# Performance work log

Hardware: AMD Instinct MI355X
Metric: run time of the kernel (lower is better)

## Reference

```python
import jax, jax.numpy as jnp
import numpy as np

EMBED_DIM = 2048
NUM_HEADS = 32
NUM_KV_HEADS = 8
HEAD_DIM = EMBED_DIM // NUM_HEADS  # 64
KV_DIM = HEAD_DIM * NUM_KV_HEADS   # 512
Q_PER_KV = NUM_HEADS // NUM_KV_HEADS  # 4


def setup_inputs() -> dict:
    key = jax.random.key(0)
    ks = jax.random.split(key, 9)
    s = 1.0 / np.sqrt(EMBED_DIM)
    x = jax.random.normal(ks[0], (2, 2048, EMBED_DIM), dtype=jnp.float32)
    Wq = jax.random.uniform(ks[1], (EMBED_DIM, EMBED_DIM), jnp.float32, -s, s)
    bq = jax.random.uniform(ks[2], (EMBED_DIM,), jnp.float32, -s, s)
    Wk = jax.random.uniform(ks[3], (KV_DIM, EMBED_DIM), jnp.float32, -s, s)
    bk = jax.random.uniform(ks[4], (KV_DIM,), jnp.float32, -s, s)
    Wv = jax.random.uniform(ks[5], (KV_DIM, EMBED_DIM), jnp.float32, -s, s)
    bv = jax.random.uniform(ks[6], (KV_DIM,), jnp.float32, -s, s)
    Wo = jax.random.uniform(ks[7], (EMBED_DIM, EMBED_DIM), jnp.float32, -s, s)
    bo = jax.random.uniform(ks[8], (EMBED_DIM,), jnp.float32, -s, s)
    return {"x": x, "Wq": Wq, "bq": bq, "Wk": Wk, "bk": bk,
            "Wv": Wv, "bv": bv, "Wo": Wo, "bo": bo}


def reference(x, Wq, bq, Wk, bk, Wv, bv, Wo, bo):
    B, S, E = x.shape
    # projections (torch Linear: x @ W.T + b)
    q = x @ Wq.T + bq                       # [B,S,E]
    k = x @ Wk.T + bk                       # [B,S,KV_DIM]
    v = x @ Wv.T + bv
    # [B, num_kv, q_per_kv, S, D] and [B, num_kv, S, D] -- GQA grouping
    # avoids repeat_interleave duplication while computing identical math
    q = q.reshape(B, S, NUM_KV_HEADS, Q_PER_KV, HEAD_DIM).transpose(0, 2, 3, 1, 4)
    k = k.reshape(B, S, NUM_KV_HEADS, HEAD_DIM).transpose(0, 2, 1, 3)
    v = v.reshape(B, S, NUM_KV_HEADS, HEAD_DIM).transpose(0, 2, 1, 3)
    scale = 1.0 / np.sqrt(HEAD_DIM).astype(np.float32)
    scores = jnp.einsum('bgqsd,bgtd->bgqst', q, k) * scale  # [B,G,Qpk,S,S]
    causal = jnp.triu(jnp.ones((S, S), dtype=bool), k=1)
    scores = jnp.where(causal, jnp.float32(-jnp.inf), scores)
    attn = jax.nn.softmax(scores, axis=-1)
    out = jnp.einsum('bgqst,bgtd->bgqsd', attn, v)          # [B,G,Qpk,S,D]
    # back to [B,S,E]: head order matches repeat_interleave (kv-major)
    out = out.transpose(0, 3, 1, 2, 4).reshape(B, S, E)
    return out @ Wo.T + bo
```

## Files before the change

kernel.cpp:

```cpp
#include <hip/hip_runtime.h>
#include <stdint.h>

#define EMBED  2048
#define SEQ    2048
#define BATCH  2
#define NHEADS 32
#define NKV    8
#define HDIM   64
#define KVD    512
#define MTOT   (BATCH*SEQ)
#define QKVN   (EMBED + 2*KVD)

typedef __bf16 bf16x8 __attribute__((ext_vector_type(8)));
typedef float  f32x4  __attribute__((ext_vector_type(4)));
typedef float  f32x8v __attribute__((ext_vector_type(8)));
typedef float  f32x2v __attribute__((ext_vector_type(2)));
typedef float  f32x16 __attribute__((ext_vector_type(16)));

#define QSCALE 0.18033688f
#define M2     11.541560f

static __device__ __forceinline__ unsigned short f2bf(float f) {
    union { float f; unsigned int u; } v; v.f = f;
    return (unsigned short)((v.u + 0x7fffu + ((v.u >> 16) & 1u)) >> 16);
}

static __device__ __forceinline__ void gload_lds16(const void* g, void* l) {
    __builtin_amdgcn_global_load_lds(
        (const __attribute__((address_space(1))) void*)g,
        (__attribute__((address_space(3))) void*)l, 16, 0, 0);
}

template<int N> static __device__ __forceinline__ void waitvm() {
    if constexpr (N == 2) asm volatile("s_waitcnt vmcnt(2)" ::: "memory");
    else if constexpr (N == 3) asm volatile("s_waitcnt vmcnt(3)" ::: "memory");
    else asm volatile("s_waitcnt vmcnt(4)" ::: "memory");
}

static __device__ __forceinline__ void cast4(const float* __restrict__ in,
                                             unsigned short* __restrict__ out, int i) {
    float4 f = reinterpret_cast<const float4*>(in)[i];
    ushort4 o;
    o.x = f2bf(f.x); o.y = f2bf(f.y); o.z = f2bf(f.z); o.w = f2bf(f.w);
    reinterpret_cast<ushort4*>(out)[i] = o;
}

__global__ __launch_bounds__(256)
void prep(const float* __restrict__ x,  const float* __restrict__ Wq,
          const float* __restrict__ Wk, const float* __restrict__ Wv,
          const float* __restrict__ Wo, const float* __restrict__ bq,
          const float* __restrict__ bk, const float* __restrict__ bv,
          unsigned short* __restrict__ xb, unsigned short* __restrict__ Wqkvb,
          unsigned short* __restrict__ Wob, float* __restrict__ bqkv)
{
    const int t0 = blockIdx.x * blockDim.x + threadIdx.x;
    const int st = gridDim.x * blockDim.x;
    for (int i = t0; i < (MTOT * EMBED) / 4;  i += st) cast4(x,  xb, i);
    for (int i = t0; i < (EMBED * EMBED) / 4; i += st) cast4(Wq, Wqkvb, i);
    for (int i = t0; i < (KVD * EMBED) / 4;   i += st) cast4(Wk, Wqkvb + EMBED * EMBED, i);
    for (int i = t0; i < (KVD * EMBED) / 4;   i += st) cast4(Wv, Wqkvb + (EMBED + KVD) * EMBED, i);
    for (int i = t0; i < (EMBED * EMBED) / 4; i += st) cast4(Wo, Wob, i);
    if (t0 < QKVN / 4) {
        float4 v = (t0 < EMBED / 4) ? reinterpret_cast<const float4*>(bq)[t0]
                 : (t0 < (EMBED + KVD) / 4) ? reinterpret_cast<const float4*>(bk)[t0 - EMBED / 4]
                 : reinterpret_cast<const float4*>(bv)[t0 - (EMBED + KVD) / 4];
        reinterpret_cast<float4*>(bqkv)[t0] = v;
    }
}

template<int WM, bool OUT_BF16>
__global__ __launch_bounds__(512, 1)
void gemm8p(const unsigned short* __restrict__ A,
            const unsigned short* __restrict__ B,
            const float* __restrict__ bias,
            void* __restrict__ C, int M, int N, int K)
{
    constexpr int BM    = WM * 32;
    constexpr int ASZ   = BM * 128;
    constexpr int BSZ   = 256 * 128;
    constexpr int AHALF = ASZ / 2;
    constexpr int AL    = AHALF / 8192;
    constexpr int BUFSZ = ASZ + BSZ;

    __shared__ __align__(16) char lds[2 * BUFSZ];

    const int tid = threadIdx.x;
    const int l   = tid & 63;
    const int w   = tid >> 6;
    const int wr  = w >> 2, wc = w & 3;
    const int lr15 = l & 15;
    const int lkb  = (l >> 4) * 16;

    const int nwg = gridDim.x;
    const int cpx = nwg >> 3;
    const int bid = blockIdx.x;
    const int swz = (bid & 7) * cpx + (bid >> 3);
    const int NMB = M / BM;
    const int m0  = (swz % NMB) * BM;
    const int n0  = (swz / NMB) * 256;

    unsigned offA[2][AL], dA[2][AL];
#pragma unroll
    for (int q = 0; q < 2; ++q)
#pragma unroll
        for (int j = 0; j < AL; ++j) {
            int L  = q * AHALF + (tid + j * 512) * 16;
            int R  = L >> 7;
            int cb = (L & 127) ^ ((R & 7) << 4);
            int lrow;
            if constexpr (WM == 8) lrow = ((R >> 6) & 1) * 128 + (R >> 7) * 64 + (R & 63);
            else                   lrow = ((R >> 5) & 1) * 64  + (R >> 6) * 32 + (R & 31);
            offA[q][j] = (unsigned)((m0 + lrow) * K * 2 + cb);
            dA[q][j]   = (unsigned)L;
        }
    unsigned offB[2][2], dB[2][2];
#pragma unroll
    for (int q = 0; q < 2; ++q)
#pragma unroll
        for (int j = 0; j < 2; ++j) {
            int L  = q * 16384 + (tid + j * 512) * 16;
            int R  = L >> 7;
            int cb = (L & 127) ^ ((R & 7) << 4);
            int lrow = ((R >> 5) & 3) * 64 + (R >> 7) * 32 + (R & 31);
            offB[q][j] = (unsigned)((n0 + lrow) * K * 2 + cb);
            dB[q][j]   = (unsigned)(ASZ + L);
        }

#define STAGE_A(q, bw, ku) { _Pragma("unroll") \
    for (int j_ = 0; j_ < AL; ++j_) \
        gload_lds16((const char*)A + offA[q][j_] + (unsigned)(ku) * 128u, (bw) + dA[q][j_]); }
#define STAGE_B(q, bw, ku) { _Pragma("unroll") \
    for (int j_ = 0; j_ < 2; ++j_) \
        gload_lds16((const char*)B + offB[q][j_] + (unsigned)(ku) * 128u, (bw) + dB[q][j_]); }

    auto rdA = [&](const char* br, int mi, int kk) -> bf16x8 {
        int row;
        if constexpr (WM == 8) row = (mi >> 2) * 128 + wr * 64 + (mi & 3) * 16 + lr15;
        else                   row = (mi >> 1) * 64  + wr * 32 + (mi & 1) * 16 + lr15;
        int byte = (row * 128 + kk * 64 + lkb) ^ ((row & 7) << 4);
        return *reinterpret_cast<const bf16x8*>(br + byte);
    };
    auto rdB = [&](const char* br, int ni, int kk) -> bf16x8 {
        int row  = (ni >> 1) * 128 + wc * 32 + (ni & 1) * 16 + lr15;
        int byte = (row * 128 + kk * 64 + lkb) ^ ((row & 7) << 4);
        return *reinterpret_cast<const bf16x8*>(br + ASZ + byte);
    };

    f32x4 acc[WM][4] = {};
    bf16x8 afr[WM / 2][2], bf0[2][2], bf1[2][2];

    STAGE_A(0, lds, 0); STAGE_B(0, lds, 0); STAGE_B(1, lds, 0); STAGE_A(1, lds, 0);
    waitvm<2 + AL>();
    __builtin_amdgcn_s_barrier();

    const int NKT = K >> 6;
    for (int u = 0; u < NKT; ++u) {
        char* br = lds + (u & 1) * BUFSZ;
        char* bw = lds + ((u & 1) ^ 1) * BUFSZ;
        const bool pf = (u + 1 < NKT);
        const int  ku = u + 1;

        if (pf) STAGE_A(0, bw, ku);
#pragma unroll
        for (int mi = 0; mi < WM / 2; ++mi)
#pragma unroll
            for (int kk = 0; kk < 2; ++kk) afr[mi][kk] = rdA(br, mi, kk);
#pragma unroll
        for (int ni = 0; ni < 2; ++ni)
#pragma unroll
            for (int kk = 0; kk < 2; ++kk) bf0[ni][kk] = rdB(br, ni, kk);
        __builtin_amdgcn_s_barrier();
        __builtin_amdgcn_s_setprio(1);
#pragma unroll
        for (int mi = 0; mi < WM / 2; ++mi)
#pragma unroll
            for (int ni = 0; ni < 2; ++ni)
#pragma unroll
                for (int kk = 0; kk < 2; ++kk)
                    acc[mi][ni] = __builtin_amdgcn_mfma_f32_16x16x32_bf16(afr[mi][kk], bf0[ni][kk], acc[mi][ni], 0, 0, 0);
        __builtin_amdgcn_s_setprio(0);
        waitvm<2 * AL>();
        __builtin_amdgcn_s_barrier();

        if (pf) STAGE_B(0, bw, ku);
#pragma unroll
        for (int ni = 0; ni < 2; ++ni)
#pragma unroll
            for (int kk = 0; kk < 2; ++kk) bf1[ni][kk] = rdB(br, 2 + ni, kk);
        __builtin_amdgcn_s_barrier();
        __builtin_amdgcn_s_setprio(1);
#pragma unroll
        for (int mi = 0; mi < WM / 2; ++mi)
#pragma unroll
            for (int ni = 0; ni < 2; ++ni)
#pragma unroll
                for (int kk = 0; kk < 2; ++kk)
                    acc[mi][2 + ni] = __builtin_amdgcn_mfma_f32_16x16x32_bf16(afr[mi][kk], bf1[ni][kk], acc[mi][2 + ni], 0, 0, 0);
        __builtin_amdgcn_s_setprio(0);
        waitvm<AL + 2>();
        __builtin_amdgcn_s_barrier();

        if (pf) STAGE_B(1, bw, ku);
#pragma unroll
        for (int mi = 0; mi < WM / 2; ++mi)
#pragma unroll
            for (int kk = 0; kk < 2; ++kk) afr[mi][kk] = rdA(br, WM / 2 + mi, kk);
        __builtin_amdgcn_s_barrier();
        __builtin_amdgcn_s_setprio(1);
#pragma unroll
        for (int mi = 0; mi < WM / 2; ++mi)
#pragma unroll
            for (int ni = 0; ni < 2; ++ni)
#pragma unroll
                for (int kk = 0; kk < 2; ++kk)
                    acc[WM / 2 + mi][ni] = __builtin_amdgcn_mfma_f32_16x16x32_bf16(afr[mi][kk], bf0[ni][kk], acc[WM / 2 + mi][ni], 0, 0, 0);
        __builtin_amdgcn_s_setprio(0);
        __builtin_amdgcn_s_barrier();

        if (pf) STAGE_A(1, bw, ku);
        __builtin_amdgcn_s_barrier();
        __builtin_amdgcn_s_setprio(1);
#pragma unroll
        for (int mi = 0; mi < WM / 2; ++mi)
#pragma unroll
            for (int ni = 0; ni < 2; ++ni)
#pragma unroll
                for (int kk = 0; kk < 2; ++kk)
                    acc[WM / 2 + mi][2 + ni] = __builtin_amdgcn_mfma_f32_16x16x32_bf16(afr[mi][kk], bf1[ni][kk], acc[WM / 2 + mi][2 + ni], 0, 0, 0);
        __builtin_amdgcn_s_setprio(0);
        waitvm<2 + AL>();
        __builtin_amdgcn_s_barrier();
    }
#undef STAGE_A
#undef STAGE_B

    float bv[4];
#pragma unroll
    for (int ni = 0; ni < 4; ++ni) bv[ni] = bias[n0 + wc * 64 + ni * 16 + lr15];
#pragma unroll
    for (int mi = 0; mi < WM; ++mi)
#pragma unroll
        for (int ni = 0; ni < 4; ++ni)
#pragma unroll
            for (int r = 0; r < 4; ++r) {
                int row = m0 + wr * (WM * 16) + mi * 16 + (l >> 4) * 4 + r;
                int col = n0 + wc * 64 + ni * 16 + lr15;
                float v = acc[mi][ni][r] + bv[ni];
                if constexpr (OUT_BF16)
                    ((unsigned short*)C)[(size_t)row * N + col] = f2bf(v);
                else
                    ((float*)C)[(size_t)row * N + col] = v;
            }
}

static __device__ __forceinline__ bf16x8 pack_frag(float p0, float p1, float p2, float p3,
                                                   float p4, float p5, float p6, float p7) {
    unsigned int w0, w1, w2, w3;
    asm("v_cvt_pk_bf16_f32 %0, %1, %2" : "=v"(w0) : "v"(p0), "v"(p1));
    asm("v_cvt_pk_bf16_f32 %0, %1, %2" : "=v"(w1) : "v"(p2), "v"(p3));
    asm("v_cvt_pk_bf16_f32 %0, %1, %2" : "=v"(w2) : "v"(p4), "v"(p5));
    asm("v_cvt_pk_bf16_f32 %0, %1, %2" : "=v"(w3) : "v"(p6), "v"(p7));
    asm("v_permlane32_swap_b32 %0, %1" : "+v"(w0), "+v"(w2));
    asm("v_permlane32_swap_b32 %0, %1" : "+v"(w1), "+v"(w3));
    union { unsigned int u[4]; bf16x8 v; } uu;
    uu.u[0] = w0; uu.u[1] = w1; uu.u[2] = w2; uu.u[3] = w3;
    return uu.v;
}

static __device__ __forceinline__ float hsum32(f32x16 a, f32x16 b) {
    f32x16 t = a + b;
    f32x8v u = __builtin_shufflevector(t, t, 0,1,2,3,4,5,6,7)
             + __builtin_shufflevector(t, t, 8,9,10,11,12,13,14,15);
    f32x4 v4 = __builtin_shufflevector(u, u, 0,1,2,3)
             + __builtin_shufflevector(u, u, 4,5,6,7);
    f32x2v v2 = __builtin_shufflevector(v4, v4, 0,1)
              + __builtin_shufflevector(v4, v4, 2,3);
    return v2[0] + v2[1];
}

static __device__ __forceinline__ void attn_tile(
    const char* __restrict__ KsBuf, const char* __restrict__ VtBuf,
    const bf16x8* qf, int q, int t0, bool diag,
    f32x16& acc0, f32x16& acc1, float& l_run,
    int lq, int hi)
{
    f32x16 s0 = {}, s1 = {};
    __builtin_amdgcn_s_setprio(1);
#pragma unroll
    for (int ks = 0; ks < 4; ++ks) {
        const int colb = (ks * 16 + hi * 8) * 2;
        int a0 = (lq * 128 + colb) ^ ((lq & 7) << 4);
        bf16x8 kf0 = *reinterpret_cast<const bf16x8*>(KsBuf + a0);
        s0 = __builtin_amdgcn_mfma_f32_32x32x16_bf16(kf0, qf[ks], s0, 0, 0, 0);
        int r1 = 32 + lq;
        int a1 = (r1 * 128 + colb) ^ ((r1 & 7) << 4);
        bf16x8 kf1 = *reinterpret_cast<const bf16x8*>(KsBuf + a1);
        s1 = __builtin_amdgcn_mfma_f32_32x32x16_bf16(kf1, qf[ks], s1, 0, 0, 0);
    }
    __builtin_amdgcn_s_setprio(0);

    if (diag) {
#pragma unroll
        for (int r = 0; r < 16; ++r) {
            int tg = t0 + (r & 3) + 8 * (r >> 2) + 4 * hi;
            if (tg > q) s0[r] = -1e30f;
            if (tg + 32 > q) s1[r] = -1e30f;
        }
    }

    s0 = s0 - M2;
    s1 = s1 - M2;
#pragma unroll
    for (int r = 0; r < 16; ++r) {
        s0[r] = __builtin_amdgcn_exp2f(s0[r]);
        s1[r] = __builtin_amdgcn_exp2f(s1[r]);
    }

    float rs = hsum32(s0, s1);
    l_run += rs + __shfl_xor(rs, 32);

    bf16x8 pa[4];
    pa[0] = pack_frag(s0[0], s0[1], s0[2], s0[3], s0[4], s0[5], s0[6], s0[7]);
    pa[1] = pack_frag(s0[8], s0[9], s0[10], s0[11], s0[12], s0[13], s0[14], s0[15]);
    pa[2] = pack_frag(s1[0], s1[1], s1[2], s1[3], s1[4], s1[5], s1[6], s1[7]);
    pa[3] = pack_frag(s1[8], s1[9], s1[10], s1[11], s1[12], s1[13], s1[14], s1[15]);

    __builtin_amdgcn_s_setprio(1);
#pragma unroll
    for (int ks = 0; ks < 4; ++ks) {
        const int colb = (ks * 16 + hi * 8) * 2;
        int a0 = (lq * 128 + colb) ^ ((lq & 7) << 4);
        bf16x8 vf0 = *reinterpret_cast<const bf16x8*>(VtBuf + a0);
        acc0 = __builtin_amdgcn_mfma_f32_32x32x16_bf16(pa[ks], vf0, acc0, 0, 0, 0);
        int d1 = 32 + lq;
        int a1 = (d1 * 128 + colb) ^ ((d1 & 7) << 4);
        bf16x8 vf1 = *reinterpret_cast<const bf16x8*>(VtBuf + a1);
        acc1 = __builtin_amdgcn_mfma_f32_32x32x16_bf16(pa[ks], vf1, acc1, 0, 0, 0);
    }
    __builtin_amdgcn_s_setprio(0);
}

__global__ __launch_bounds__(256, 2)
void gqa_attn(const unsigned short* __restrict__ qkv,
              unsigned short* __restrict__ ctx)
{
    __shared__ __align__(16) unsigned short Ks[2][64 * 64];
    __shared__ __align__(16) unsigned short Vt[2][64 * 64];

    const int bid = blockIdx.x;
    const int g   = bid & 7;
    const int bh  = (bid >> 3) & 3;
    const int b   = bh >> 1;
    const int hp  = bh & 1;
    const int qt  = 31 - (bid >> 5);
    const int NT  = qt + 1;

    const int tid = threadIdx.x;
    const int l   = tid & 63;
    const int w   = tid >> 6;
    const int hi  = l >> 5;
    const int lq  = l & 31;

    const int h   = g * 4 + hp * 2 + (w >> 1);
    const int q0  = qt * 64 + (w & 1) * 32;
    const size_t rowb = (size_t)b * SEQ;
    const int kbase = EMBED + g * HDIM;
    const int vbase = EMBED + KVD + g * HDIM;

    bf16x8 qf[4];
    {
        const char* qa = (const char*)qkv + ((rowb + q0 + lq) * QKVN + (size_t)h * HDIM) * 2;
#pragma unroll
        for (int ks = 0; ks < 4; ++ks) {
            bf16x8 ta = *reinterpret_cast<const bf16x8*>(qa + (ks * 16 + hi * 8) * 2);
#pragma unroll
            for (int j = 0; j < 8; ++j)
                ta[j] = (__bf16)((float)ta[j] * QSCALE);
            qf[ks] = ta;
        }
    }

    f32x16 acc0 = {}, acc1 = {};
    float l_run = 0.0f;

    const int Lk0 = tid << 4;
    const int Lk1 = (tid + 256) << 4;
    const int Tk0 = Lk0 ^ (((Lk0 >> 7) & 7) << 4);
    const int Tk1 = Lk1 ^ (((Lk1 >> 7) & 7) << 4);
    const int kr0 = Tk0 >> 7, ko0 = Tk0 & 127;
    const int kr1 = Tk1 >> 7, ko1 = Tk1 & 127;

    const int vd0 = w * 16;

    {
        gload_lds16((const char*)qkv + ((rowb + kr0) * QKVN + kbase) * 2 + ko0, (char*)Ks[0] + Lk0);
        gload_lds16((const char*)qkv + ((rowb + kr1) * QKVN + kbase) * 2 + ko1, (char*)Ks[0] + Lk1);
        const char* vp = (const char*)qkv + ((rowb + l) * QKVN + vbase + vd0) * 2;
        uint4 v0 = *reinterpret_cast<const uint4*>(vp);
        uint4 v1 = *reinterpret_cast<const uint4*>(vp + 16);
        const unsigned short* e0 = (const unsigned short*)&v0;
        const unsigned short* e1 = (const unsigned short*)&v1;
#pragma unroll
        for (int j = 0; j < 8; ++j) {
            int d0 = vd0 + j, d1 = vd0 + 8 + j;
            *(unsigned short*)((char*)Vt[0] + ((d0 * 128 + l * 2) ^ ((d0 & 7) << 4))) = e0[j];
            *(unsigned short*)((char*)Vt[0] + ((d1 * 128 + l * 2) ^ ((d1 & 7) << 4))) = e1[j];
        }
    }
    __syncthreads();

    for (int kt = 0; kt < NT; ++kt) {
        const int cur = kt & 1;
        const int t0  = kt * 64;
        const bool haveNext = (kt + 1 < NT);
        uint4 vn0, vn1;
        if (haveNext) {
            gload_lds16((const char*)qkv + ((rowb + t0 + 64 + kr0) * QKVN + kbase) * 2 + ko0,
                        (char*)Ks[cur ^ 1] + Lk0);
            gload_lds16((const char*)qkv + ((rowb + t0 + 64 + kr1) * QKVN + kbase) * 2 + ko1,
                        (char*)Ks[cur ^ 1] + Lk1);
            const char* vp = (const char*)qkv + ((rowb + t0 + 64 + l) * QKVN + vbase + vd0) * 2;
            vn0 = *reinterpret_cast<const uint4*>(vp);
            vn1 = *reinterpret_cast<const uint4*>(vp + 16);
        }

        attn_tile((const char*)Ks[cur], (const char*)Vt[cur], qf, q0 + lq, t0,
                  kt == qt, acc0, acc1, l_run, lq, hi);

        if (haveNext) {
            const unsigned short* e0 = (const unsigned short*)&vn0;
            const unsigned short* e1 = (const unsigned short*)&vn1;
#pragma unroll
            for (int j = 0; j < 8; ++j) {
                int d0 = vd0 + j, d1 = vd0 + 8 + j;
                *(unsigned short*)((char*)Vt[cur ^ 1] + ((d0 * 128 + l * 2) ^ ((d0 & 7) << 4))) = e0[j];
                *(unsigned short*)((char*)Vt[cur ^ 1] + ((d1 * 128 + l * 2) ^ ((d1 & 7) << 4))) = e1[j];
            }
            __syncthreads();
        }
    }

#pragma unroll
    for (int r = 0; r < 16; ++r) {
        int qr  = (r & 3) + 8 * (r >> 2) + 4 * hi;
        int col = h * HDIM + lq;
        float lr = __shfl(l_run, qr);
        size_t row = rowb + q0 + qr;
        ctx[row * EMBED + col]      = f2bf(acc0[r] / lr);
        ctx[row * EMBED + col + 32] = f2bf(acc1[r] / lr);
    }
}

extern "C" void kernel_launch(void* const* d_in, const int* in_sizes, int n_in,
                              void* d_out, int out_size, void* d_ws, size_t ws_size,
                              hipStream_t stream) {
    (void)in_sizes; (void)n_in; (void)out_size; (void)ws_size;
    const float* x  = (const float*)d_in[0];
    const float* Wq = (const float*)d_in[1];
    const float* bq = (const float*)d_in[2];
    const float* Wk = (const float*)d_in[3];
    const float* bk = (const float*)d_in[4];
    const float* Wv = (const float*)d_in[5];
    const float* bv = (const float*)d_in[6];
    const float* Wo = (const float*)d_in[7];
    const float* bo = (const float*)d_in[8];
    float* out = (float*)d_out;

    char* ws = (char*)d_ws;
    unsigned short* xb    = (unsigned short*)(ws);
    unsigned short* Wqkvb = (unsigned short*)(ws + 16777216);
    unsigned short* Wob   = (unsigned short*)(ws + 29360128);
    float*          bqkv  = (float*)         (ws + 37748736);
    unsigned short* QKVb  = (unsigned short*)(ws + 37761024);
    unsigned short* ctx   = (unsigned short*)(ws + 62926848);

    prep<<<2048, 256, 0, stream>>>(x, Wq, Wk, Wv, Wo, bq, bk, bv,
                                   xb, Wqkvb, Wob, bqkv);

    gemm8p<8, true><<<dim3(192), 512, 0, stream>>>(
        xb, Wqkvb, bqkv, QKVb, MTOT, QKVN, EMBED);

    gqa_attn<<<dim3(1024), 256, 0, stream>>>(QKVb, ctx);

    gemm8p<4, false><<<dim3(256), 512, 0, stream>>>(
        ctx, Wob, bo, out, MTOT, EMBED, EMBED);
}
```

Measured before the change: 175.6 us.

## Pre-transpose V into global buffer and load it asynchronously into LDS

Adds a separate kernel that transposes V from the fused QKV buffer into a per-(batch, kv-group) [D, S] layout, reusing the no-longer-needed xb workspace. The attention kernel then stages V tiles with the same direct global-to-LDS async loads and swizzle as K, replacing per-thread register loads followed by scalar 2-byte scattered LDS writes. The aim is to remove the costly transpose scatter from the attention inner loop and let V prefetch overlap compute. It costs an extra kernel launch and an extra read and write of V through global memory.

```diff
diff --git a/kernel.cpp b/kernel.cpp
--- a/kernel.cpp
+++ b/kernel.cpp
@@ -68,6 +68,34 @@
     }
 }
 
+__global__ __launch_bounds__(256)
+void transpose_v(const unsigned short* __restrict__ qkv,
+                 unsigned short* __restrict__ vt)
+{
+    __shared__ __align__(16) unsigned short T[64][72];
+    const int bg = blockIdx.x & 15;
+    const int bt = blockIdx.x >> 4;
+    const int b  = bg >> 3, g = bg & 7;
+    const int tid = threadIdx.x;
+    const int tr  = tid >> 2, c = tid & 3;
+
+    const unsigned short* src = qkv + ((size_t)(b * SEQ + bt * 64 + tr)) * QKVN
+                              + (EMBED + KVD) + g * HDIM + c * 16;
+    uint4 v0 = *reinterpret_cast<const uint4*>(src);
+    uint4 v1 = *reinterpret_cast<const uint4*>(src + 8);
+    *reinterpret_cast<uint4*>(&T[tr][c * 16])     = v0;
+    *reinterpret_cast<uint4*>(&T[tr][c * 16 + 8]) = v1;
+    __syncthreads();
+
+    const int dr = tr;
+    unsigned short o[16];
+#pragma unroll
+    for (int j = 0; j < 16; ++j) o[j] = T[c * 16 + j][dr];
+    unsigned short* dst = vt + ((size_t)(bg * 64 + dr)) * SEQ + bt * 64 + c * 16;
+    *reinterpret_cast<uint4*>(dst)     = *reinterpret_cast<uint4*>(o);
+    *reinterpret_cast<uint4*>(dst + 8) = *reinterpret_cast<uint4*>(o + 8);
+}
+
 template<int WM, bool OUT_BF16>
 __global__ __launch_bounds__(512, 1)
 void gemm8p(const unsigned short* __restrict__ A,
@@ -278,74 +306,13 @@
     return v2[0] + v2[1];
 }
 
-static __device__ __forceinline__ void attn_tile(
-    const char* __restrict__ KsBuf, const char* __restrict__ VtBuf,
-    const bf16x8* qf, int q, int t0, bool diag,
-    f32x16& acc0, f32x16& acc1, float& l_run,
-    int lq, int hi)
-{
-    f32x16 s0 = {}, s1 = {};
-    __builtin_amdgcn_s_setprio(1);
-#pragma unroll
-    for (int ks = 0; ks < 4; ++ks) {
-        const int colb = (ks * 16 + hi * 8) * 2;
-        int a0 = (lq * 128 + colb) ^ ((lq & 7) << 4);
-        bf16x8 kf0 = *reinterpret_cast<const bf16x8*>(KsBuf + a0);
-        s0 = __builtin_amdgcn_mfma_f32_32x32x16_bf16(kf0, qf[ks], s0, 0, 0, 0);
-        int r1 = 32 + lq;
-        int a1 = (r1 * 128 + colb) ^ ((r1 & 7) << 4);
-        bf16x8 kf1 = *reinterpret_cast<const bf16x8*>(KsBuf + a1);
-        s1 = __builtin_amdgcn_mfma_f32_32x32x16_bf16(kf1, qf[ks], s1, 0, 0, 0);
-    }
-    __builtin_amdgcn_s_setprio(0);
-
-    if (diag) {
-#pragma unroll
-        for (int r = 0; r < 16; ++r) {
-            int tg = t0 + (r & 3) + 8 * (r >> 2) + 4 * hi;
-            if (tg > q) s0[r] = -1e30f;
-            if (tg + 32 > q) s1[r] = -1e30f;
-        }
-    }
-
-    s0 = s0 - M2;
-    s1 = s1 - M2;
-#pragma unroll
-    for (int r = 0; r < 16; ++r) {
-        s0[r] = __builtin_amdgcn_exp2f(s0[r]);
-        s1[r] = __builtin_amdgcn_exp2f(s1[r]);
-    }
-
-    float rs = hsum32(s0, s1);
-    l_run += rs + __shfl_xor(rs, 32);
-
-    bf16x8 pa[4];
-    pa[0] = pack_frag(s0[0], s0[1], s0[2], s0[3], s0[4], s0[5], s0[6], s0[7]);
-    pa[1] = pack_frag(s0[8], s0[9], s0[10], s0[11], s0[12], s0[13], s0[14], s0[15]);
-    pa[2] = pack_frag(s1[0], s1[1], s1[2], s1[3], s1[4], s1[5], s1[6], s1[7]);
-    pa[3] = pack_frag(s1[8], s1[9], s1[10], s1[11], s1[12], s1[13], s1[14], s1[15]);
-
-    __builtin_amdgcn_s_setprio(1);
-#pragma unroll
-    for (int ks = 0; ks < 4; ++ks) {
-        const int colb = (ks * 16 + hi * 8) * 2;
-        int a0 = (lq * 128 + colb) ^ ((lq & 7) << 4);
-        bf16x8 vf0 = *reinterpret_cast<const bf16x8*>(VtBuf + a0);
-        acc0 = __builtin_amdgcn_mfma_f32_32x32x16_bf16(pa[ks], vf0, acc0, 0, 0, 0);
-        int d1 = 32 + lq;
-        int a1 = (d1 * 128 + colb) ^ ((d1 & 7) << 4);
-        bf16x8 vf1 = *reinterpret_cast<const bf16x8*>(VtBuf + a1);
-        acc1 = __builtin_amdgcn_mfma_f32_32x32x16_bf16(pa[ks], vf1, acc1, 0, 0, 0);
-    }
-    __builtin_amdgcn_s_setprio(0);
-}
-
 __global__ __launch_bounds__(256, 2)
 void gqa_attn(const unsigned short* __restrict__ qkv,
+              const unsigned short* __restrict__ vtg,
               unsigned short* __restrict__ ctx)
 {
     __shared__ __align__(16) unsigned short Ks[2][64 * 64];
-    __shared__ __align__(16) unsigned short Vt[2][64 * 64];
+    __shared__ __align__(16) unsigned short Vs[2][64 * 64];
 
     const int bid = blockIdx.x;
     const int g   = bid & 7;
@@ -365,7 +332,6 @@
     const int q0  = qt * 64 + (w & 1) * 32;
     const size_t rowb = (size_t)b * SEQ;
     const int kbase = EMBED + g * HDIM;
-    const int vbase = EMBED + KVD + g * HDIM;
 
     bf16x8 qf[4];
     {
@@ -390,55 +356,84 @@
     const int kr0 = Tk0 >> 7, ko0 = Tk0 & 127;
     const int kr1 = Tk1 >> 7, ko1 = Tk1 & 127;
 
-    const int vd0 = w * 16;
-
-    {
-        gload_lds16((const char*)qkv + ((rowb + kr0) * QKVN + kbase) * 2 + ko0, (char*)Ks[0] + Lk0);
-        gload_lds16((const char*)qkv + ((rowb + kr1) * QKVN + kbase) * 2 + ko1, (char*)Ks[0] + Lk1);
-        const char* vp = (const char*)qkv + ((rowb + l) * QKVN + vbase + vd0) * 2;
-        uint4 v0 = *reinterpret_cast<const uint4*>(vp);
-        uint4 v1 = *reinterpret_cast<const uint4*>(vp + 16);
-        const unsigned short* e0 = (const unsigned short*)&v0;
-        const unsigned short* e1 = (const unsigned short*)&v1;
-#pragma unroll
-        for (int j = 0; j < 8; ++j) {
-            int d0 = vd0 + j, d1 = vd0 + 8 + j;
-            *(unsigned short*)((char*)Vt[0] + ((d0 * 128 + l * 2) ^ ((d0 & 7) << 4))) = e0[j];
-            *(unsigned short*)((char*)Vt[0] + ((d1 * 128 + l * 2) ^ ((d1 & 7) << 4))) = e1[j];
-        }
-    }
+    const char* vtb = (const char*)vtg + (size_t)(b * 8 + g) * HDIM * SEQ * 2;
+
+#define STAGE_KV(buf, tt) { \
+    gload_lds16((const char*)qkv + ((rowb + (tt) + kr0) * QKVN + kbase) * 2 + ko0, (char*)Ks[buf] + Lk0); \
+    gload_lds16((const char*)qkv + ((rowb + (tt) + kr1) * QKVN + kbase) * 2 + ko1, (char*)Ks[buf] + Lk1); \
+    gload_lds16(vtb + ((size_t)kr0 * SEQ + (tt)) * 2 + ko0, (char*)Vs[buf] + Lk0); \
+    gload_lds16(vtb + ((size_t)kr1 * SEQ + (tt)) * 2 + ko1, (char*)Vs[buf] + Lk1); }
+
+    STAGE_KV(0, 0);
     __syncthreads();
 
     for (int kt = 0; kt < NT; ++kt) {
         const int cur = kt & 1;
         const int t0  = kt * 64;
         const bool haveNext = (kt + 1 < NT);
-        uint4 vn0, vn1;
-        if (haveNext) {
-            gload_lds16((const char*)qkv + ((rowb + t0 + 64 + kr0) * QKVN + kbase) * 2 + ko0,
-                        (char*)Ks[cur ^ 1] + Lk0);
-            gload_lds16((const char*)qkv + ((rowb + t0 + 64 + kr1) * QKVN + kbase) * 2 + ko1,
-                        (char*)Ks[cur ^ 1] + Lk1);
-            const char* vp = (const char*)qkv + ((rowb + t0 + 64 + l) * QKVN + vbase + vd0) * 2;
-            vn0 = *reinterpret_cast<const uint4*>(vp);
-            vn1 = *reinterpret_cast<const uint4*>(vp + 16);
-        }
-
-        attn_tile((const char*)Ks[cur], (const char*)Vt[cur], qf, q0 + lq, t0,
-                  kt == qt, acc0, acc1, l_run, lq, hi);
-
-        if (haveNext) {
-            const unsigned short* e0 = (const unsigned short*)&vn0;
-            const unsigned short* e1 = (const unsigned short*)&vn1;
-#pragma unroll
-            for (int j = 0; j < 8; ++j) {
-                int d0 = vd0 + j, d1 = vd0 + 8 + j;
-                *(unsigned short*)((char*)Vt[cur ^ 1] + ((d0 * 128 + l * 2) ^ ((d0 & 7) << 4))) = e0[j];
-                *(unsigned short*)((char*)Vt[cur ^ 1] + ((d1 * 128 + l * 2) ^ ((d1 & 7) << 4))) = e1[j];
+        if (haveNext) STAGE_KV(cur ^ 1, t0 + 64);
+
+        const char* KsBuf = (const char*)Ks[cur];
+        f32x16 s0 = {}, s1 = {};
+        __builtin_amdgcn_s_setprio(1);
+#pragma unroll
+        for (int ks = 0; ks < 4; ++ks) {
+            const int colb = (ks * 16 + hi * 8) * 2;
+            int a0 = (lq * 128 + colb) ^ ((lq & 7) << 4);
+            bf16x8 kf0 = *reinterpret_cast<const bf16x8*>(KsBuf + a0);
+            s0 = __builtin_amdgcn_mfma_f32_32x32x16_bf16(kf0, qf[ks], s0, 0, 0, 0);
+            int r1 = 32 + lq;
+            int a1 = (r1 * 128 + colb) ^ ((r1 & 7) << 4);
+            bf16x8 kf1 = *reinterpret_cast<const bf16x8*>(KsBuf + a1);
+            s1 = __builtin_amdgcn_mfma_f32_32x32x16_bf16(kf1, qf[ks], s1, 0, 0, 0);
+        }
+        __builtin_amdgcn_s_setprio(0);
+
+        if (kt == qt) {
+            const int q = q0 + lq;
+#pragma unroll
+            for (int r = 0; r < 16; ++r) {
+                int tg = t0 + (r & 3) + 8 * (r >> 2) + 4 * hi;
+                if (tg > q) s0[r] = -1e30f;
+                if (tg + 32 > q) s1[r] = -1e30f;
             }
-            __syncthreads();
-        }
+        }
+
+        s0 = s0 - M2;
+        s1 = s1 - M2;
+#pragma unroll
+        for (int r = 0; r < 16; ++r) {
+            s0[r] = __builtin_amdgcn_exp2f(s0[r]);
+            s1[r] = __builtin_amdgcn_exp2f(s1[r]);
+        }
+
+        float rs = hsum32(s0, s1);
+        l_run += rs + __shfl_xor(rs, 32);
+
+        bf16x8 pa[4];
+        pa[0] = pack_frag(s0[0], s0[1], s0[2], s0[3], s0[4], s0[5], s0[6], s0[7]);
+        pa[1] = pack_frag(s0[8], s0[9], s0[10], s0[11], s0[12], s0[13], s0[14], s0[15]);
+        pa[2] = pack_frag(s1[0], s1[1], s1[2], s1[3], s1[4], s1[5], s1[6], s1[7]);
+        pa[3] = pack_frag(s1[8], s1[9], s1[10], s1[11], s1[12], s1[13], s1[14], s1[15]);
+
+        const char* VsBuf = (const char*)Vs[cur];
+        __builtin_amdgcn_s_setprio(1);
+#pragma unroll
+        for (int ks = 0; ks < 4; ++ks) {
+            const int colb = (ks * 16 + hi * 8) * 2;
+            int a0 = (lq * 128 + colb) ^ ((lq & 7) << 4);
+            bf16x8 vf0 = *reinterpret_cast<const bf16x8*>(VsBuf + a0);
+            acc0 = __builtin_amdgcn_mfma_f32_32x32x16_bf16(pa[ks], vf0, acc0, 0, 0, 0);
+            int d1 = 32 + lq;
+            int a1 = (d1 * 128 + colb) ^ ((d1 & 7) << 4);
+            bf16x8 vf1 = *reinterpret_cast<const bf16x8*>(VsBuf + a1);
+            acc1 = __builtin_amdgcn_mfma_f32_32x32x16_bf16(pa[ks], vf1, acc1, 0, 0, 0);
+        }
+        __builtin_amdgcn_s_setprio(0);
+
+        if (haveNext) __syncthreads();
     }
+#undef STAGE_KV
 
 #pragma unroll
     for (int r = 0; r < 16; ++r) {
@@ -473,6 +468,7 @@
     float*          bqkv  = (float*)         (ws + 37748736);
     unsigned short* QKVb  = (unsigned short*)(ws + 37761024);
     unsigned short* ctx   = (unsigned short*)(ws + 62926848);
+    unsigned short* VT    = xb;
 
     prep<<<2048, 256, 0, stream>>>(x, Wq, Wk, Wv, Wo, bq, bk, bv,
                                    xb, Wqkvb, Wob, bqkv);
@@ -480,7 +476,9 @@
     gemm8p<8, true><<<dim3(192), 512, 0, stream>>>(
         xb, Wqkvb, bqkv, QKVb, MTOT, QKVN, EMBED);
 
-    gqa_attn<<<dim3(1024), 256, 0, stream>>>(QKVb, ctx);
+    transpose_v<<<dim3(512), 256, 0, stream>>>(QKVb, VT);
+
+    gqa_attn<<<dim3(1024), 256, 0, stream>>>(QKVb, VT, ctx);
 
     gemm8p<4, false><<<dim3(256), 512, 0, stream>>>(
         ctx, Wob, bo, out, MTOT, EMBED, EMBED);
```

New measurement: 170.4 us. 3.0% less time.
